# Optimization experiments

Hardware: AMD Instinct MI355X
Metric: run time of the kernel (lower is better)

The kernel has to match this reference:

```python
import math
import jax, jax.numpy as jnp
import numpy as np

D_MODEL = 1024
N_HEADS = 16
HEAD_DIM = D_MODEL // N_HEADS
B, L = 1, 4096


def _slopes(n_heads):
    ratio = 2.0 ** (-8.0 / n_heads)
    return jnp.asarray([ratio ** (i + 1) for i in range(n_heads)], dtype=jnp.float32)


def setup_inputs() -> dict:
    key = jax.random.key(0)
    ks = jax.random.split(key, 5)
    scale = 1.0 / math.sqrt(D_MODEL)
    return {
        "x": jax.random.normal(ks[0], (B, L, D_MODEL), dtype=jnp.float32),
        "q_w": jax.random.normal(ks[1], (D_MODEL, D_MODEL), dtype=jnp.float32) * scale,
        "k_w": jax.random.normal(ks[2], (D_MODEL, D_MODEL), dtype=jnp.float32) * scale,
        "v_w": jax.random.normal(ks[3], (D_MODEL, D_MODEL), dtype=jnp.float32) * scale,
        "o_w": jax.random.normal(ks[4], (D_MODEL, D_MODEL), dtype=jnp.float32) * scale,
    }


def reference(x, q_w, k_w, v_w, o_w):
    b, l, _ = x.shape
    # projections -> [B, H, L, hd]
    def proj(w):
        return (x @ w).reshape(b, l, N_HEADS, HEAD_DIM).transpose(0, 2, 1, 3)
    q, k, v = proj(q_w), proj(k_w), proj(v_w)

    scale = math.sqrt(HEAD_DIM)
    scores = jnp.einsum("bhid,bhjd->bhij", q, k) / scale  # [B,H,L,L]

    pos = jnp.arange(l)
    distance = jnp.abs(pos[None, :] - pos[:, None]).astype(jnp.float32)  # [L,L]
    alibi = -distance[None, :, :] * _slopes(N_HEADS)[:, None, None]       # [H,L,L]
    scores = scores + alibi[None]

    causal = pos[None, :] <= pos[:, None]  # j <= i
    scores = jnp.where(causal[None, None], scores, -jnp.inf)

    attn = jax.nn.softmax(scores, axis=-1)
    out = jnp.einsum("bhij,bhjd->bhid", attn, v)
    out = out.transpose(0, 2, 1, 3).reshape(b, l, D_MODEL)
    return out @ o_w
```

## Files before the change

kernel.cpp:

```cpp
#include <hip/hip_runtime.h>

#define L_SEQ 4096
#define DM    1024
#define NH    16
#define HD    64

typedef unsigned short ushort_t;
typedef __attribute__((ext_vector_type(8))) short bf16x8;
typedef __attribute__((ext_vector_type(4))) float f32x4;

__device__ inline unsigned short f2bf(float f) {
    union { float f; unsigned int u; } v; v.f = f;
    unsigned int r = v.u + 0x7fffu + ((v.u >> 16) & 1u);
    return (unsigned short)(r >> 16);
}

__device__ inline unsigned cvt_pk_bf16(float lo, float hi) {
    unsigned w;
    asm("v_cvt_pk_bf16_f32 %0, %1, %2" : "=v"(w) : "v"(lo), "v"(hi));
    return w;
}

__device__ inline float ex2(float x) {
#if __has_builtin(__builtin_amdgcn_exp2f)
    return __builtin_amdgcn_exp2f(x);
#else
    return exp2f(x);
#endif
}

__device__ inline void load_lds16(const ushort_t* g, ushort_t* l) {
    __builtin_amdgcn_global_load_lds(
        (const __attribute__((address_space(1))) unsigned int*)g,
        (__attribute__((address_space(3))) unsigned int*)l, 16, 0, 0);
}

__device__ inline bool detect_f32(const ushort_t* xraw) {
    __shared__ int s_flag;
    const int t = threadIdx.x;
    if (t < 64) {
        unsigned e = (xraw[2 * t] >> 7) & 0xFFu;
        unsigned long long m = __ballot(e >= 0x88u);
        if (t == 0) s_flag = (__popcll(m) >= 8) ? 1 : 0;
    }
    __syncthreads();
    return s_flag != 0;
}

__global__ __launch_bounds__(256) void convert_all(const void* __restrict__ xv,
                                                   const void* __restrict__ w0,
                                                   const void* __restrict__ w1,
                                                   const void* __restrict__ w2,
                                                   const void* __restrict__ w3,
                                                   ushort_t* __restrict__ xb,
                                                   ushort_t* __restrict__ wT) {
    bool f32 = detect_f32((const ushort_t*)xv);
    const int z = blockIdx.z;
    const int t = threadIdx.x;

    if (z == 4) {
        const int B0 = (blockIdx.y * 16 + blockIdx.x) * 16384;
        #pragma unroll
        for (int it = 0; it < 8; ++it) {
            const int i = B0 + it * 2048 + t * 8;
            if (f32) {
                const float* xf = (const float*)xv;
                float4 v0 = *(const float4*)(xf + i);
                float4 v1 = *(const float4*)(xf + i + 4);
                uint4 u;
                u.x = cvt_pk_bf16(v0.x, v0.y);
                u.y = cvt_pk_bf16(v0.z, v0.w);
                u.z = cvt_pk_bf16(v1.x, v1.y);
                u.w = cvt_pk_bf16(v1.z, v1.w);
                *(uint4*)(xb + i) = u;
            } else {
                *(uint4*)(xb + i) = *(const uint4*)((const ushort_t*)xv + i);
            }
        }
        return;
    }

    const void* w = (z == 0) ? w0 : (z == 1) ? w1 : (z == 2) ? w2 : w3;
    ushort_t* out = wT + (size_t)z * (DM * DM);
    __shared__ ushort_t T[64][65];
    const int k0 = blockIdx.x * 64, n0 = blockIdx.y * 64;
    #pragma unroll
    for (int i = 0; i < 16; ++i) {
        int e = t + i * 256;
        int r = e >> 6, c = e & 63;
        T[r][c] = f32 ? f2bf(((const float*)w)[(size_t)(k0 + r) * DM + n0 + c])
                      : ((const ushort_t*)w)[(size_t)(k0 + r) * DM + n0 + c];
    }
    __syncthreads();
    #pragma unroll
    for (int i = 0; i < 16; ++i) {
        int e = t + i * 256;
        int d = e >> 6, l = e & 63;
        out[(size_t)(n0 + d) * DM + k0 + l] = T[l][d];
    }
}

__device__ inline void gemm128_body(const ushort_t* __restrict__ A,
                                    const ushort_t* __restrict__ Bt,
                                    void* __restrict__ Cv, int cmode,
                                    int m0, int n0) {
    constexpr int K = 1024, NOUT = 1024;
    __shared__ ushort_t As[128 * 64];
    __shared__ ushort_t Bs[128 * 64];

    const int t = threadIdx.x, lane = t & 63, wave = t >> 6;
    const int l15 = lane & 15, quad = lane >> 4;
    const int mw = (wave >> 1) * 64, nw = (wave & 1) * 64;
    const int srow = lane >> 3;
    const int sgr  = (lane & 7) ^ (lane >> 3);
    const int swz  = l15 & 7;

    f32x4 acc[4][4] = {};

    for (int k0 = 0; k0 < K; k0 += 64) {
        #pragma unroll
        for (int i = 0; i < 4; ++i) {
            const int j = wave * 4 + i;
            load_lds16(A  + (size_t)(m0 + 8 * j + srow) * K + k0 + sgr * 8,
                       &As[8 * j * 64]);
            load_lds16(Bt + (size_t)(n0 + 8 * j + srow) * K + k0 + sgr * 8,
                       &Bs[8 * j * 64]);
        }
        __syncthreads();

        #pragma unroll
        for (int kt = 0; kt < 2; ++kt) {
            bf16x8 af[4], bf[4];
            #pragma unroll
            for (int i = 0; i < 4; ++i) {
                af[i] = *(const bf16x8*)&As[(mw + i * 16 + l15) * 64
                                            + (((kt * 4 + quad) ^ swz) * 8)];
                bf[i] = *(const bf16x8*)&Bs[(nw + i * 16 + l15) * 64
                                            + (((kt * 4 + quad) ^ swz) * 8)];
            }
            #pragma unroll
            for (int mt = 0; mt < 4; ++mt)
                #pragma unroll
                for (int nt = 0; nt < 4; ++nt)
                    acc[mt][nt] = __builtin_amdgcn_mfma_f32_16x16x32_bf16(
                        af[mt], bf[nt], acc[mt][nt], 0, 0, 0);
        }
        __syncthreads();
    }

    if (cmode == 2) {
        ushort_t* Vt = (ushort_t*)Cv;
        #pragma unroll
        for (int mt = 0; mt < 4; ++mt)
            #pragma unroll
            for (int nt = 0; nt < 4; ++nt) {
                int col  = n0 + nw + nt * 16 + l15;
                int row0 = m0 + mw + mt * 16 + quad * 4;
                ushort_t pk[4] = {f2bf(acc[mt][nt][0]), f2bf(acc[mt][nt][1]),
                                  f2bf(acc[mt][nt][2]), f2bf(acc[mt][nt][3])};
                *(uint2*)&Vt[(size_t)col * L_SEQ + row0] = *(const uint2*)pk;
            }
        return;
    }

    const int odd = lane & 1;
    #pragma unroll
    for (int mtp = 0; mtp < 2; ++mtp)
        #pragma unroll
        for (int nt = 0; nt < 4; ++nt)
            #pragma unroll
            for (int r = 0; r < 4; ++r) {
                float zA = acc[2 * mtp][nt][r];
                float zB = acc[2 * mtp + 1][nt][r];
                float send = odd ? zA : zB;
                float got  = __shfl_xor(send, 1);
                const int row = m0 + mw + (2 * mtp + odd) * 16 + quad * 4 + r;
                const int col = n0 + nw + nt * 16 + (l15 & ~1);
                if (cmode == 1) {
                    float2 w2 = odd ? make_float2(got, zB) : make_float2(zA, got);
                    *(float2*)((float*)Cv + (size_t)row * NOUT + col) = w2;
                } else {
                    float lo = odd ? got : zA;
                    float hi = odd ? zB  : got;
                    unsigned w = cvt_pk_bf16(lo, hi);
                    *(unsigned*)((ushort_t*)Cv + (size_t)row * NOUT + col) = w;
                }
            }
}

__global__ __launch_bounds__(256) void qkv128(const ushort_t* __restrict__ xb,
                                              const ushort_t* __restrict__ wT,
                                              ushort_t* Qp, ushort_t* Kp, ushort_t* Vt) {
    const int b = blockIdx.x;
    const int n0 = (b & 7) * 128;
    const int u  = b >> 3;
    const int m0 = (u / 3) * 128;
    const int z  = u % 3;
    const ushort_t* Bt = wT + (size_t)z * (DM * DM);
    if (z == 0)      gemm128_body(xb, Bt, Qp, 0, m0, n0);
    else if (z == 1) gemm128_body(xb, Bt, Kp, 0, m0, n0);
    else             gemm128_body(xb, Bt, Vt, 2, m0, n0);
}

__global__ __launch_bounds__(256) void ogemm128(const void* __restrict__ xdet,
                                                const ushort_t* __restrict__ An,
                                                const ushort_t* __restrict__ woT,
                                                void* __restrict__ C) {
    bool f32 = detect_f32((const ushort_t*)xdet);
    const int b = blockIdx.x;
    const int n0 = (b & 7) * 128, m0 = (b >> 3) * 128;
    gemm128_body(An, woT, C, f32 ? 1 : 0, m0, n0);
}

__global__ __launch_bounds__(512) void attn_kernel(const ushort_t* __restrict__ Q,
                                                   const ushort_t* __restrict__ Kp,
                                                   const ushort_t* __restrict__ Vt,
                                                   ushort_t* __restrict__ O) {
    __shared__ ushort_t Ks[2][128 * 64];
    __shared__ ushort_t Vs[2][64 * 128];
    __shared__ ushort_t Pt[128 * 128];

    const int b    = blockIdx.x;
    const int h    = 2 * (b & 7) + ((b >> 3) & 1);
    const int px   = b >> 4;
    const int t    = threadIdx.x;
    const int lane = t & 63, wave = t >> 6;
    const int l15  = lane & 15, quad = lane >> 4;
    const float LOG2E  = 1.44269504f;
    const float slope2 = exp2f(-0.5f * (float)(h + 1)) * LOG2E;
    const float c0     = 0.125f * LOG2E;
    const float qd4f   = (float)(quad * 4);

    const int krow = lane >> 3, kgr = (lane & 7) ^ (lane >> 3);
    const int vsub = lane >> 4;
    const int swz = l15 & 7;

    auto stage_load = [&](int buf, int kv0) {
        #pragma unroll
        for (int i = 0; i < 2; ++i) {
            const int j = wave * 2 + i;
            const int r = 8 * j + krow;
            load_lds16(Kp + (size_t)(kv0 + r) * DM + h * HD + kgr * 8,
                       &Ks[buf][8 * j * 64]);
        }
        #pragma unroll
        for (int i = 0; i < 2; ++i) {
            const int j = wave * 2 + i;
            const int d = 4 * j + vsub;
            const int g = (lane & 15) ^ (4 * (j & 1) + vsub);
            load_lds16(Vt + (size_t)(h * HD + d) * L_SEQ + kv0 + g * 8,
                       &Vs[buf][4 * j * 128]);
        }
    };

    int par = 0;
    stage_load(0, 0);

    #pragma unroll
    for (int half = 0; half < 2; ++half) {
        const int qb = half ? px : (31 - px);
        const int q0 = qb * 128;
        const int qg = q0 + wave * 16 + l15;
        const float qf = (float)qg;
        const int nst = half ? (px + 1) : (32 - px);

        bf16x8 bq[2];
        #pragma unroll
        for (int kt = 0; kt < 2; ++kt)
            bq[kt] = *(const bf16x8*)(Q + (size_t)qg * DM + h * HD + kt * 32 + quad * 8);

        f32x4 acc_o[4] = {};
        float l_r = 0.f;

        for (int s = 0; s < nst; ++s) {
            const int kv0 = s * 128;
            __syncthreads();

            const int nkv0 = (s + 1 < nst) ? (s + 1) * 128 : 0;
            stage_load(par ^ 1, nkv0);

            f32x4 sacc[8];
            #pragma unroll
            for (int mt = 0; mt < 8; ++mt) sacc[mt] = (f32x4){0.f, 0.f, 0.f, 0.f};
            __builtin_amdgcn_s_setprio(1);
            #pragma unroll
            for (int kt = 0; kt < 2; ++kt)
                #pragma unroll
                for (int mt = 0; mt < 8; ++mt) {
                    bf16x8 a = *(const bf16x8*)&Ks[par][(mt * 16 + l15) * 64
                                                        + (((kt * 4 + quad) ^ swz) * 8)];
                    sacc[mt] = __builtin_amdgcn_mfma_f32_16x16x32_bf16(a, bq[kt], sacc[mt], 0, 0, 0);
                }
            __builtin_amdgcn_s_setprio(0);

            const bool diag = (kv0 + 128 > q0);
            const float off = slope2 * ((float)kv0 + qd4f - qf);
            float rs = 0.f;
            #pragma unroll
            for (int mt = 0; mt < 8; ++mt)
                #pragma unroll
                for (int r = 0; r < 4; ++r) {
                    float kvl = (float)(mt * 16 + r);
                    float s2  = fmaf(sacc[mt][r], c0, fmaf(slope2, kvl, off));
                    if (diag) {
                        int kvg = kv0 + mt * 16 + quad * 4 + r;
                        s2 = (kvg <= qg) ? s2 : -1e30f;
                    }
                    float p = ex2(s2);
                    sacc[mt][r] = p;
                    rs += p;
                }
            rs += __shfl_xor(rs, 16);
            rs += __shfl_xor(rs, 32);
            l_r += rs;

            #pragma unroll
            for (int mt = 0; mt < 8; ++mt) {
                union { float f; unsigned u; } a0, a1, a2, a3;
                a0.f = sacc[mt][0]; a1.f = sacc[mt][1];
                a2.f = sacc[mt][2]; a3.f = sacc[mt][3];
                uint2 w;
                w.x = __builtin_amdgcn_perm(a1.u, a0.u, 0x07060302);
                w.y = __builtin_amdgcn_perm(a3.u, a2.u, 0x07060302);
                const int g = mt * 2 + (quad >> 1);
                *(uint2*)&Pt[(wave * 16 + l15) * 128
                             + ((g ^ swz) * 8 + (quad & 1) * 4)] = w;
            }
            __threadfence_block();

            __builtin_amdgcn_s_setprio(1);
            #pragma unroll
            for (int kt = 0; kt < 4; ++kt) {
                bf16x8 a = *(const bf16x8*)&Pt[(wave * 16 + l15) * 128
                                               + (((kt * 4 + quad) ^ swz) * 8)];
                #pragma unroll
                for (int nt = 0; nt < 4; ++nt) {
                    bf16x8 bvv = *(const bf16x8*)&Vs[par][(nt * 16 + l15) * 128
                                                          + (((kt * 4 + quad) ^ swz) * 8)];
                    acc_o[nt] = __builtin_amdgcn_mfma_f32_16x16x32_bf16(a, bvv, acc_o[nt], 0, 0, 0);
                }
            }
            __builtin_amdgcn_s_setprio(0);

            par ^= 1;
        }

        float linv[4];
        #pragma unroll
        for (int r = 0; r < 4; ++r) linv[r] = 1.0f / __shfl(l_r, quad * 4 + r);
        #pragma unroll
        for (int nt = 0; nt < 4; ++nt)
            #pragma unroll
            for (int r = 0; r < 4; ++r) {
                int row = q0 + wave * 16 + quad * 4 + r;
                O[(size_t)row * DM + h * HD + nt * 16 + l15] = f2bf(acc_o[nt][r] * linv[r]);
            }
    }
}

extern "C" void kernel_launch(void* const* d_in, const int* in_sizes, int n_in,
                              void* d_out, int out_size, void* d_ws, size_t ws_size,
                              hipStream_t stream) {
    const void* x  = d_in[0];
    const void* wq = d_in[1];
    const void* wk = d_in[2];
    const void* wv = d_in[3];
    const void* wo = d_in[4];

    const size_t SZ = (size_t)L_SEQ * DM;
    const size_t WZ = (size_t)DM * DM;
    ushort_t* xb = (ushort_t*)d_ws;
    ushort_t* wT = xb + SZ;
    ushort_t* Qp = wT + 4 * WZ;
    ushort_t* Kp = Qp + SZ;
    ushort_t* Vt = Kp + SZ;
    ushort_t* An = xb;

    convert_all<<<dim3(16, 16, 5), 256, 0, stream>>>(x, wq, wk, wv, wo, xb, wT);
    qkv128<<<768, 256, 0, stream>>>(xb, wT, Qp, Kp, Vt);
    attn_kernel<<<256, 512, 0, stream>>>(Qp, Kp, Vt, An);
    ogemm128<<<256, 256, 0, stream>>>(x, An, wT + 3 * WZ, d_out);
}
```

Baseline: 232.5 us.

## Split attention KV range across two blocks and add combine kernel

Adds a split-KV attention kernel in which each of two blocks per (head, query-pair) handles alternating 128-wide KV tiles and writes unnormalized fp32 partial outputs and row sums. A separate combine kernel sums the two partials, normalizes and converts to bf16. The aim is to double the grid from 256 to 512 blocks for better CU occupancy on the GPU. In exchange it adds fp32 partial traffic, an extra launch, and drops double-buffered K/V prefetch. It only runs when the workspace is large enough.

```diff
diff --git a/kernel.cpp b/kernel.cpp
--- a/kernel.cpp
+++ b/kernel.cpp
@@ -239,8 +239,7 @@
         #pragma unroll
         for (int i = 0; i < 2; ++i) {
             const int j = wave * 2 + i;
-            const int r = 8 * j + krow;
-            load_lds16(Kp + (size_t)(kv0 + r) * DM + h * HD + kgr * 8,
+            load_lds16(Kp + (size_t)(kv0 + 8 * j + krow) * DM + h * HD + kgr * 8,
                        &Ks[buf][8 * j * 64]);
         }
         #pragma unroll
@@ -358,6 +357,172 @@
     }
 }
 
+__global__ __launch_bounds__(512, 4) void attn_split(const ushort_t* __restrict__ Q,
+                                                     const ushort_t* __restrict__ Kp,
+                                                     const ushort_t* __restrict__ Vt,
+                                                     float* __restrict__ Op,
+                                                     float* __restrict__ Lp) {
+    __shared__ ushort_t Ks[128 * 64];
+    __shared__ ushort_t Vs[64 * 128];
+    __shared__ ushort_t Pt[128 * 128];
+
+    const int b    = blockIdx.x;
+    const int bb   = b & 255;
+    const int v    = b >> 8;
+    const int h    = 2 * (bb & 7) + ((bb >> 3) & 1);
+    const int px   = bb >> 4;
+    const int t    = threadIdx.x;
+    const int lane = t & 63, wave = t >> 6;
+    const int l15  = lane & 15, quad = lane >> 4;
+    const float LOG2E  = 1.44269504f;
+    const float slope2 = exp2f(-0.5f * (float)(h + 1)) * LOG2E;
+    const float c0     = 0.125f * LOG2E;
+    const float qd4f   = (float)(quad * 4);
+
+    const int krow = lane >> 3, kgr = (lane & 7) ^ (lane >> 3);
+    const int vsub = lane >> 4;
+    const int swz = l15 & 7;
+
+    float* Opv = Op + (size_t)v * L_SEQ * DM;
+
+    auto stage_load = [&](int kv0) {
+        #pragma unroll
+        for (int i = 0; i < 2; ++i) {
+            const int j = wave * 2 + i;
+            load_lds16(Kp + (size_t)(kv0 + 8 * j + krow) * DM + h * HD + kgr * 8,
+                       &Ks[8 * j * 64]);
+        }
+        #pragma unroll
+        for (int i = 0; i < 2; ++i) {
+            const int j = wave * 2 + i;
+            const int d = 4 * j + vsub;
+            const int g = (lane & 15) ^ (4 * (j & 1) + vsub);
+            load_lds16(Vt + (size_t)(h * HD + d) * L_SEQ + kv0 + g * 8,
+                       &Vs[4 * j * 128]);
+        }
+    };
+
+    #pragma unroll
+    for (int half = 0; half < 2; ++half) {
+        const int qb = half ? px : (31 - px);
+        const int q0 = qb * 128;
+        const int qg = q0 + wave * 16 + l15;
+        const float qf = (float)qg;
+        const int nst = half ? (px + 1) : (32 - px);
+
+        bf16x8 bq[2];
+        #pragma unroll
+        for (int kt = 0; kt < 2; ++kt)
+            bq[kt] = *(const bf16x8*)(Q + (size_t)qg * DM + h * HD + kt * 32 + quad * 8);
+
+        f32x4 acc_o[4] = {};
+        float l_r = 0.f;
+
+        for (int s = v; s < nst; s += 2) {
+            const int kv0 = s * 128;
+            stage_load(kv0);
+            __syncthreads();
+
+            f32x4 sacc[8];
+            #pragma unroll
+            for (int mt = 0; mt < 8; ++mt) sacc[mt] = (f32x4){0.f, 0.f, 0.f, 0.f};
+            __builtin_amdgcn_s_setprio(1);
+            #pragma unroll
+            for (int kt = 0; kt < 2; ++kt)
+                #pragma unroll
+                for (int mt = 0; mt < 8; ++mt) {
+                    bf16x8 a = *(const bf16x8*)&Ks[(mt * 16 + l15) * 64
+                                                   + (((kt * 4 + quad) ^ swz) * 8)];
+                    sacc[mt] = __builtin_amdgcn_mfma_f32_16x16x32_bf16(a, bq[kt], sacc[mt], 0, 0, 0);
+                }
+            __builtin_amdgcn_s_setprio(0);
+
+            const bool diag = (kv0 + 128 > q0);
+            const float off = slope2 * ((float)kv0 + qd4f - qf);
+            float rs = 0.f;
+            #pragma unroll
+            for (int mt = 0; mt < 8; ++mt)
+                #pragma unroll
+                for (int r = 0; r < 4; ++r) {
+                    float kvl = (float)(mt * 16 + r);
+                    float s2  = fmaf(sacc[mt][r], c0, fmaf(slope2, kvl, off));
+                    if (diag) {
+                        int kvg = kv0 + mt * 16 + quad * 4 + r;
+                        s2 = (kvg <= qg) ? s2 : -1e30f;
+                    }
+                    float p = ex2(s2);
+                    sacc[mt][r] = p;
+                    rs += p;
+                }
+            rs += __shfl_xor(rs, 16);
+            rs += __shfl_xor(rs, 32);
+            l_r += rs;
+
+            #pragma unroll
+            for (int mt = 0; mt < 8; ++mt) {
+                union { float f; unsigned u; } a0, a1, a2, a3;
+                a0.f = sacc[mt][0]; a1.f = sacc[mt][1];
+                a2.f = sacc[mt][2]; a3.f = sacc[mt][3];
+                uint2 w;
+                w.x = __builtin_amdgcn_perm(a1.u, a0.u, 0x07060302);
+                w.y = __builtin_amdgcn_perm(a3.u, a2.u, 0x07060302);
+                const int g = mt * 2 + (quad >> 1);
+                *(uint2*)&Pt[(wave * 16 + l15) * 128
+                             + ((g ^ swz) * 8 + (quad & 1) * 4)] = w;
+            }
+            __threadfence_block();
+
+            __builtin_amdgcn_s_setprio(1);
+            #pragma unroll
+            for (int kt = 0; kt < 4; ++kt) {
+                bf16x8 a = *(const bf16x8*)&Pt[(wave * 16 + l15) * 128
+                                               + (((kt * 4 + quad) ^ swz) * 8)];
+                #pragma unroll
+                for (int nt = 0; nt < 4; ++nt) {
+                    bf16x8 bvv = *(const bf16x8*)&Vs[(nt * 16 + l15) * 128
+                                                     + (((kt * 4 + quad) ^ swz) * 8)];
+                    acc_o[nt] = __builtin_amdgcn_mfma_f32_16x16x32_bf16(a, bvv, acc_o[nt], 0, 0, 0);
+                }
+            }
+            __builtin_amdgcn_s_setprio(0);
+
+            __syncthreads();
+        }
+
+        #pragma unroll
+        for (int nt = 0; nt < 4; ++nt)
+            #pragma unroll
+            for (int r = 0; r < 4; ++r) {
+                int row = q0 + wave * 16 + quad * 4 + r;
+                Opv[(size_t)row * DM + h * HD + nt * 16 + l15] = acc_o[nt][r];
+            }
+        if (quad == 0)
+            Lp[(size_t)v * (NH * L_SEQ) + (size_t)h * L_SEQ + qg] = l_r;
+    }
+}
+
+__global__ __launch_bounds__(256) void attn_combine(const float* __restrict__ Op,
+                                                    const float* __restrict__ Lp,
+                                                    ushort_t* __restrict__ An) {
+    const int i = (blockIdx.x * 256 + threadIdx.x) * 8;
+    const int row = i >> 10;
+    const int h   = (i & 1023) >> 6;
+    const float l0 = Lp[(size_t)h * L_SEQ + row];
+    const float l1 = Lp[(size_t)NH * L_SEQ + (size_t)h * L_SEQ + row];
+    const float linv = 1.0f / (l0 + l1);
+    const size_t V1 = (size_t)L_SEQ * DM;
+    float4 a0 = *(const float4*)(Op + i);
+    float4 a1 = *(const float4*)(Op + i + 4);
+    float4 b0 = *(const float4*)(Op + V1 + i);
+    float4 b1 = *(const float4*)(Op + V1 + i + 4);
+    uint4 u;
+    u.x = cvt_pk_bf16((a0.x + b0.x) * linv, (a0.y + b0.y) * linv);
+    u.y = cvt_pk_bf16((a0.z + b0.z) * linv, (a0.w + b0.w) * linv);
+    u.z = cvt_pk_bf16((a1.x + b1.x) * linv, (a1.y + b1.y) * linv);
+    u.w = cvt_pk_bf16((a1.z + b1.z) * linv, (a1.w + b1.w) * linv);
+    *(uint4*)(An + i) = u;
+}
+
 extern "C" void kernel_launch(void* const* d_in, const int* in_sizes, int n_in,
                               void* d_out, int out_size, void* d_ws, size_t ws_size,
                               hipStream_t stream) {
@@ -376,8 +541,17 @@
     ushort_t* Vt = Kp + SZ;
     ushort_t* An = xb;
 
+    float* Op = (float*)(Vt + SZ);
+    float* Lp = Op + 2 * SZ;
+    const size_t need = 40ull * 1024 * 1024 + 2 * SZ * 4 + 2ull * NH * L_SEQ * 4;
+
     convert_all<<<dim3(16, 16, 5), 256, 0, stream>>>(x, wq, wk, wv, wo, xb, wT);
     qkv128<<<768, 256, 0, stream>>>(xb, wT, Qp, Kp, Vt);
-    attn_kernel<<<256, 512, 0, stream>>>(Qp, Kp, Vt, An);
+    if (ws_size >= need) {
+        attn_split<<<512, 512, 0, stream>>>(Qp, Kp, Vt, Op, Lp);
+        attn_combine<<<2048, 256, 0, stream>>>(Op, Lp, An);
+    } else {
+        attn_kernel<<<256, 512, 0, stream>>>(Qp, Kp, Vt, An);
+    }
     ogemm128<<<256, 256, 0, stream>>>(x, An, wT + 3 * WZ, d_out);
 }
```

Measured after the change: 221.7 us (median of 2 runs). 1.05x faster.
